# Optimization experiments

Hardware: AMD Instinct MI355X
Metric: run time of the kernel (lower is better)

## Reference

```python
import jax, jax.numpy as jnp
import numpy as np

NUM_VIDEOS = 1024       # B
SECTIONS_PER_VIDEO = 32 # avg segment length (uniform here for simplicity)
NUM_CLASSES = 1024      # C
TOTAL_SECTIONS = NUM_VIDEOS * SECTIONS_PER_VIDEO
EPS = 1e-4


def setup_inputs() -> dict:
    key = jax.random.key(0)
    k1, k2, k3 = jax.random.split(key, 3)
    # scores are probabilities (module uses BCELoss directly on them)
    section_scores = jax.random.uniform(k1, (TOTAL_SECTIONS, NUM_CLASSES),
                                        minval=EPS, maxval=1.0 - EPS, dtype=jnp.float32)
    video_scores = jax.random.uniform(k2, (NUM_VIDEOS, NUM_CLASSES),
                                      minval=EPS, maxval=1.0 - EPS, dtype=jnp.float32)
    labels = (jax.random.uniform(k3, (NUM_VIDEOS, NUM_CLASSES)) > 0.5).astype(jnp.float32)
    # flat encoding of the ragged `segments` list: section i belongs to video segment_ids[i]
    segment_ids = jnp.repeat(jnp.arange(NUM_VIDEOS, dtype=jnp.int32), SECTIONS_PER_VIDEO)
    return {"section_scores": section_scores, "video_scores": video_scores,
            "labels": labels, "segment_ids": segment_ids}


def _bce(p, y):
    # torch.nn.BCELoss(reduction='mean'): mean over all elements
    return -jnp.mean(y * jnp.log(p) + (1.0 - y) * jnp.log1p(-p))


def reference(section_scores, video_scores, labels, segment_ids):
    # fused ragged per-video max-reduce over sections (replaces the Python loop)
    video_scores_from_sections = jax.ops.segment_max(
        section_scores, segment_ids, num_segments=NUM_VIDEOS)  # [B, C]
    video_loss = _bce(video_scores, labels)
    video_loss_from_sections = _bce(video_scores_from_sections, labels)
    return video_loss + video_loss_from_sections
```

## Files before the change

kernel.cpp:

```cpp
#include <hip/hip_runtime.h>


#define NUM_VIDEOS   1024
#define SECS_PER_VID 32
#define NUM_CLASSES  1024

__global__ __launch_bounds__(256) void hloss_kernel(
    const float* __restrict__ sec,
    const float* __restrict__ vid,
    const float* __restrict__ lab,
    float* __restrict__ out)
{
    const int v = blockIdx.x;
    const int t = threadIdx.x;

    const float4* secv = reinterpret_cast<const float4*>(sec + (size_t)v * SECS_PER_VID * NUM_CLASSES) + t;
    const float4* vidv = reinterpret_cast<const float4*>(vid + (size_t)v * NUM_CLASSES) + t;
    const float4* labv = reinterpret_cast<const float4*>(lab + (size_t)v * NUM_CLASSES) + t;

    float4 m = secv[0];
    #pragma unroll
    for (int r = 1; r < SECS_PER_VID; ++r) {
        float4 x = secv[r * (NUM_CLASSES / 4)];
        m.x = fmaxf(m.x, x.x);
        m.y = fmaxf(m.y, x.y);
        m.z = fmaxf(m.z, x.z);
        m.w = fmaxf(m.w, x.w);
    }

    float4 p = *vidv;
    float4 y = *labv;

    float qpx = (y.x > 0.5f) ? p.x : (1.0f - p.x);
    float qpy = (y.y > 0.5f) ? p.y : (1.0f - p.y);
    float qpz = (y.z > 0.5f) ? p.z : (1.0f - p.z);
    float qpw = (y.w > 0.5f) ? p.w : (1.0f - p.w);
    float qmx = (y.x > 0.5f) ? m.x : (1.0f - m.x);
    float qmy = (y.y > 0.5f) ? m.y : (1.0f - m.y);
    float qmz = (y.z > 0.5f) ? m.z : (1.0f - m.z);
    float qmw = (y.w > 0.5f) ? m.w : (1.0f - m.w);

    float prod = ((qpx * qmx) * (qpy * qmy)) * ((qpz * qmz) * (qpw * qmw));
    float s = -__logf(prod);

    #pragma unroll
    for (int off = 32; off >= 1; off >>= 1)
        s += __shfl_down(s, off, 64);

    __shared__ float wsum[4];
    const int wave = t >> 6;
    const int lane = t & 63;
    if (lane == 0) wsum[wave] = s;
    __syncthreads();
    if (t == 0) {
        const float inv = 1.0f / ((float)NUM_VIDEOS * (float)NUM_CLASSES);
        atomicAdd(out, (wsum[0] + wsum[1] + wsum[2] + wsum[3]) * inv);
    }
}

extern "C" void kernel_launch(void* const* d_in, const int* in_sizes, int n_in,
                              void* d_out, int out_size, void* d_ws, size_t ws_size,
                              hipStream_t stream) {
    const float* sec = (const float*)d_in[0];
    const float* vid = (const float*)d_in[1];
    const float* lab = (const float*)d_in[2];

    float* out = (float*)d_out;

    hipMemsetAsync(out, 0, sizeof(float), stream);
    hloss_kernel<<<NUM_VIDEOS, 256, 0, stream>>>(sec, vid, lab, out);
}
```

Baseline: 34.43 us.

## Replace memset and atomicAdd with flag-synchronized last-block reduction

Drops the separate hipMemsetAsync launch and the per-block float atomicAdd. Each block now writes its partial sum to workspace and publishes a release flag. The final block spin-waits on all flags, sums the partials in double, resets the flags and writes the output. The video-score and label loads are also issued before the section max loop. This relies on all blocks being co-resident and on the workspace flags starting at zero. The final block's serialized wait adds tail latency.

```diff
diff --git a/kernel.cpp b/kernel.cpp
--- a/kernel.cpp
+++ b/kernel.cpp
@@ -4,19 +4,24 @@
 #define NUM_VIDEOS   1024
 #define SECS_PER_VID 32
 #define NUM_CLASSES  1024
+#define FLAG_MAGIC   0x5A17C0DEu
+#define FINAL_BLOCK  (NUM_VIDEOS - 1)
 
-__global__ __launch_bounds__(256) void hloss_kernel(
+__global__ __launch_bounds__(256) void hloss_fused_kernel(
     const float* __restrict__ sec,
     const float* __restrict__ vid,
     const float* __restrict__ lab,
+    float* __restrict__ partials,
+    unsigned* __restrict__ flags,
     float* __restrict__ out)
 {
     const int v = blockIdx.x;
     const int t = threadIdx.x;
 
     const float4* secv = reinterpret_cast<const float4*>(sec + (size_t)v * SECS_PER_VID * NUM_CLASSES) + t;
-    const float4* vidv = reinterpret_cast<const float4*>(vid + (size_t)v * NUM_CLASSES) + t;
-    const float4* labv = reinterpret_cast<const float4*>(lab + (size_t)v * NUM_CLASSES) + t;
+
+    float4 p = reinterpret_cast<const float4*>(vid + (size_t)v * NUM_CLASSES)[t];
+    float4 y = reinterpret_cast<const float4*>(lab + (size_t)v * NUM_CLASSES)[t];
 
     float4 m = secv[0];
     #pragma unroll
@@ -27,9 +32,6 @@
         m.z = fmaxf(m.z, x.z);
         m.w = fmaxf(m.w, x.w);
     }
-
-    float4 p = *vidv;
-    float4 y = *labv;
 
     float qpx = (y.x > 0.5f) ? p.x : (1.0f - p.x);
     float qpy = (y.y > 0.5f) ? p.y : (1.0f - p.y);
@@ -53,8 +55,33 @@
     if (lane == 0) wsum[wave] = s;
     __syncthreads();
     if (t == 0) {
-        const float inv = 1.0f / ((float)NUM_VIDEOS * (float)NUM_CLASSES);
-        atomicAdd(out, (wsum[0] + wsum[1] + wsum[2] + wsum[3]) * inv);
+        partials[v] = (wsum[0] + wsum[1]) + (wsum[2] + wsum[3]);
+        __hip_atomic_store(&flags[v], FLAG_MAGIC, __ATOMIC_RELEASE,
+                           __HIP_MEMORY_SCOPE_AGENT);
+    }
+
+    if (v == FINAL_BLOCK && t < 64) {
+        double d = 0.0;
+        #pragma unroll
+        for (int i = 0; i < NUM_VIDEOS / 64; ++i) {
+            const int idx = lane + 64 * i;
+            while (__hip_atomic_load(&flags[idx], __ATOMIC_ACQUIRE,
+                                     __HIP_MEMORY_SCOPE_AGENT) != FLAG_MAGIC)
+                __builtin_amdgcn_s_sleep(8);
+            d += (double)partials[idx];
+        }
+
+        #pragma unroll
+        for (int off = 32; off >= 1; off >>= 1)
+            d += __shfl_down(d, off, 64);
+
+        #pragma unroll
+        for (int i = 0; i < NUM_VIDEOS / 64; ++i)
+            __hip_atomic_store(&flags[lane + 64 * i], 0u, __ATOMIC_RELAXED,
+                               __HIP_MEMORY_SCOPE_AGENT);
+
+        if (lane == 0)
+            out[0] = (float)(d / (double)((size_t)NUM_VIDEOS * NUM_CLASSES));
     }
 }
 
@@ -65,8 +92,10 @@
     const float* vid = (const float*)d_in[1];
     const float* lab = (const float*)d_in[2];
 
-    float* out = (float*)d_out;
+    float*    partials = (float*)d_ws;
+    unsigned* flags    = (unsigned*)(partials + NUM_VIDEOS);
+    float*    out      = (float*)d_out;
 
-    hipMemsetAsync(out, 0, sizeof(float), stream);
-    hloss_kernel<<<NUM_VIDEOS, 256, 0, stream>>>(sec, vid, lab, out);
+    hloss_fused_kernel<<<NUM_VIDEOS, 256, 0, stream>>>(sec, vid, lab,
+                                                       partials, flags, out);
 }
```

Measured after the change: 52.40 us. +52.2%, slower.
